# Performance work log

Hardware: AMD Instinct MI355X
Metric: run time of the kernel (lower is better)

Reference implementation:

```python
import jax, jax.numpy as jnp
import numpy as np

HIDDEN = 1024
HEADS = 16
D_K = HIDDEN // HEADS
B, S = 2, 2048


def setup_inputs() -> dict:
    key = jax.random.key(0)
    ks = jax.random.split(key, 11)
    sc = 1.0 / np.sqrt(HIDDEN)
    inp = {
        "q": jax.random.normal(ks[0], (B, S, HIDDEN), jnp.float32),
        "k": jax.random.normal(ks[1], (B, S, HIDDEN), jnp.float32),
        "v": jax.random.normal(ks[2], (B, S, HIDDEN), jnp.float32),
        "Wq": jax.random.normal(ks[3], (HIDDEN, HIDDEN), jnp.float32) * sc,
        "bq": jnp.zeros((HIDDEN,), jnp.float32),
        "Wk": jax.random.normal(ks[4], (HIDDEN, HIDDEN), jnp.float32) * sc,
        "bk": jnp.zeros((HIDDEN,), jnp.float32),
        "Wv": jax.random.normal(ks[5], (HIDDEN, HIDDEN), jnp.float32) * sc,
        "bv": jnp.zeros((HIDDEN,), jnp.float32),
        "Wo": jax.random.normal(ks[6], (HIDDEN, HIDDEN), jnp.float32) * sc,
        "bo": jnp.zeros((HIDDEN,), jnp.float32),
    }
    return inp


def reference(q, k, v, Wq, bq, Wk, bk, Wv, bv, Wo, bo):
    bs = q.shape[0]
    # projections; torch Linear: x @ W.T + b
    def proj(x, W, b):
        y = x @ W.T + b  # [B,S,H*Dk]
        return y.reshape(bs, -1, HEADS, D_K).transpose(0, 2, 1, 3)  # [B,h,S,Dk]
    qh, kh, vh = proj(q, Wq, bq), proj(k, Wk, bk), proj(v, Wv, bv)
    scores = jnp.einsum("bhqd,bhkd->bhqk", qh, kh) / jnp.sqrt(jnp.float32(D_K))
    attn = jax.nn.softmax(scores, axis=-1)  # dropout is identity in eval mode
    x = jnp.einsum("bhqk,bhkd->bhqd", attn, vh)
    x = x.transpose(0, 2, 1, 3).reshape(bs, -1, HEADS * D_K)
    return x @ Wo.T + bo
```

## Files before the change

kernel.cpp:

```cpp
#include <hip/hip_runtime.h>
#include <stdint.h>

#define HIDDEN 1024
#define HEADS  16
#define DK     64
#define BATCH  2
#define SEQ    2048
#define MTOT   (BATCH*SEQ)
#define QSCALE 0.1803368801111204f

typedef float  f32x4   __attribute__((ext_vector_type(4)));
typedef float  f32x16  __attribute__((ext_vector_type(16)));
typedef __bf16 bf16x8  __attribute__((ext_vector_type(8)));

__device__ __forceinline__ unsigned short f2bf(float f) {
    union { float f; uint32_t u; } x;
    x.f = f;
    uint32_t r = x.u + 0x7fffu + ((x.u >> 16) & 1u);
    return (unsigned short)(r >> 16);
}

__device__ __forceinline__ bf16x8 ld_bf8(const unsigned short* p) {
    return *reinterpret_cast<const bf16x8*>(p);
}

__device__ __forceinline__ void gload16(const void* g, void* l) {
    __builtin_amdgcn_global_load_lds(
        (const __attribute__((address_space(1))) void*)g,
        (__attribute__((address_space(3))) void*)l, 16, 0, 0);
}

__device__ __forceinline__ uint32_t pkbf(float a, float b) {
    union { __bf16 h[2]; uint32_t u; } pk;
    pk.h[0] = (__bf16)a; pk.h[1] = (__bf16)b;
    return pk.u;
}

struct Cvt7 {
    const float* s[7];
    unsigned short* d[7];
    int n8[7];
};
__global__ __launch_bounds__(256) void cvt_all(Cvt7 a) {
    int id = blockIdx.y;
    int i = blockIdx.x * blockDim.x + threadIdx.x;
    if (i >= a.n8[id]) return;
    const float4* s = reinterpret_cast<const float4*>(a.s[id]) + (size_t)i * 2;
    float4 x = s[0], y = s[1];
    union { unsigned short us[8]; uint4 v; } o;
    o.us[0] = f2bf(x.x); o.us[1] = f2bf(x.y); o.us[2] = f2bf(x.z); o.us[3] = f2bf(x.w);
    o.us[4] = f2bf(y.x); o.us[5] = f2bf(y.y); o.us[6] = f2bf(y.z); o.us[7] = f2bf(y.w);
    reinterpret_cast<uint4*>(a.d[id])[i] = o.v;
}

__device__ __forceinline__ void gemm_body(const unsigned short* __restrict__ A,
                                          const unsigned short* __restrict__ W,
                                          const float* __restrict__ bias,
                                          void* __restrict__ out, int mode, float scale) {
    __shared__ __align__(16) unsigned short Alds[2][128 * 64];
    __shared__ __align__(16) unsigned short Blds[2][128 * 64];
    const int t    = threadIdx.x;
    const int lane = t & 63;
    const int wid  = t >> 6;
    const int wm   = (wid >> 1) * 64;
    const int wn   = (wid & 1) * 64;
    const int fr   = lane & 15;
    const int fg   = lane >> 4;
    const int bm   = blockIdx.y, bn = blockIdx.x;
    const int K    = HIDDEN;

    f32x4 acc[4][4];
#pragma unroll
    for (int i = 0; i < 4; i++)
#pragma unroll
        for (int j = 0; j < 4; j++) acc[i][j] = (f32x4){0.f, 0.f, 0.f, 0.f};

    const int seg_row = t >> 3;
    const int seg_col = ((t & 7) ^ (seg_row & 7)) * 8;
    const int ldst    = (t & ~63) * 8;

    const unsigned short* ga = A + (size_t)(bm * 128 + seg_row) * K + seg_col;
    const unsigned short* gb = W + (size_t)(bn * 128 + seg_row) * K + seg_col;

    auto stage = [&](int k0, int buf) {
#pragma unroll
        for (int i = 0; i < 4; i++) {
            gload16(ga + (size_t)(i * 32) * K + k0, &Alds[buf][i * 2048 + ldst]);
            gload16(gb + (size_t)(i * 32) * K + k0, &Blds[buf][i * 2048 + ldst]);
        }
    };

    stage(0, 0);
    __syncthreads();

    for (int ks = 0; ks < K / 64; ++ks) {
        const int cur = ks & 1;
        if (ks < K / 64 - 1) stage((ks + 1) * 64, cur ^ 1);
#pragma unroll
        for (int kk = 0; kk < 2; kk++) {
            bf16x8 af[4], bf[4];
#pragma unroll
            for (int mt = 0; mt < 4; mt++)
                af[mt] = ld_bf8(&Alds[cur][(wm + mt * 16 + fr) * 64 +
                                           (((kk * 4 + fg) ^ (fr & 7)) * 8)]);
#pragma unroll
            for (int nt = 0; nt < 4; nt++)
                bf[nt] = ld_bf8(&Blds[cur][(wn + nt * 16 + fr) * 64 +
                                           (((kk * 4 + fg) ^ (fr & 7)) * 8)]);
#pragma unroll
            for (int mt = 0; mt < 4; mt++)
#pragma unroll
                for (int nt = 0; nt < 4; nt++)
                    acc[mt][nt] = __builtin_amdgcn_mfma_f32_16x16x32_bf16(
                        af[mt], bf[nt], acc[mt][nt], 0, 0, 0);
        }
        __syncthreads();
    }

    const int base_row = bm * 128 + wm + fg * 4;
    const int base_col = bn * 128 + wn + fr;
#pragma unroll
    for (int mt = 0; mt < 4; mt++) {
#pragma unroll
        for (int nt = 0; nt < 4; nt++) {
            int col = base_col + nt * 16;
            float bv = bias[col];
#pragma unroll
            for (int e = 0; e < 4; e++) {
                int row = base_row + mt * 16 + e;
                float val = (acc[mt][nt][e] + bv) * scale;
                if (mode == 2) {
                    ((float*)out)[(size_t)row * HIDDEN + col] = val;
                } else {
                    int b = row >> 11, s = row & (SEQ - 1);
                    int h = col >> 6, d = col & (DK - 1);
                    size_t idx;
                    if (mode == 0)
                        idx = ((size_t)(b * HEADS + h) * SEQ + s) * DK + d;
                    else
                        idx = ((size_t)(b * HEADS + h) * DK + d) * SEQ + s;
                    ((unsigned short*)out)[idx] = f2bf(val);
                }
            }
        }
    }
}

__global__ __launch_bounds__(256) void gemm_qkv(
    const unsigned short* __restrict__ qbf, const unsigned short* __restrict__ kbf,
    const unsigned short* __restrict__ vbf, const unsigned short* __restrict__ wq,
    const unsigned short* __restrict__ wk, const unsigned short* __restrict__ wv,
    const float* __restrict__ bq, const float* __restrict__ bk,
    const float* __restrict__ bv, unsigned short* __restrict__ qh,
    unsigned short* __restrict__ kh, unsigned short* __restrict__ vt) {
    int z = blockIdx.z;
    const unsigned short* A = (z == 0) ? qbf : (z == 1) ? kbf : vbf;
    const unsigned short* W = (z == 0) ? wq : (z == 1) ? wk : wv;
    const float* bias       = (z == 0) ? bq : (z == 1) ? bk : bv;
    unsigned short* out     = (z == 0) ? qh : (z == 1) ? kh : vt;
    gemm_body(A, W, bias, out, (z == 2) ? 1 : 0, (z == 0) ? QSCALE : 1.0f);
}

__global__ __launch_bounds__(256) void gemm_out(const unsigned short* __restrict__ ctx,
                                                const unsigned short* __restrict__ wo,
                                                const float* __restrict__ bo,
                                                float* __restrict__ out) {
    gemm_body(ctx, wo, bo, out, 2, 1.0f);
}

__global__ __launch_bounds__(512, 4) void attn_kernel(const unsigned short* __restrict__ qh,
                                                      const unsigned short* __restrict__ kh,
                                                      const unsigned short* __restrict__ vt,
                                                      unsigned short* __restrict__ ctx) {
    const int t = threadIdx.x, lane = t & 63, w = t >> 6;
    const int lo = lane & 31, hi = lane >> 5;
    const int qsub = w & 3, split = w >> 2;
    const int id = blockIdx.x;
    const int g  = (id & 7) * 64 + (id >> 3);
    const int by = g >> 4;
    const int bx = g & 15;
    const size_t hb = (size_t)by * (SEQ * DK);
    const int q0 = bx * 128 + qsub * 32;

    struct KV { unsigned short K[2][2][64 * 64]; unsigned short V[2][2][64 * 64]; };
    struct MG { float Lo[4][32][64]; float Lml[4][2][64]; };
    __shared__ union SMem { KV kv; MG mg; } sm;

    const unsigned short* sp[4];
    unsigned short* dpK[4];
    int sstr[4];
#pragma unroll
    for (int i = 0; i < 4; ++i) {
        int u   = w * 4 + i;
        int isV = u >> 4;
        int ssp = (u >> 3) & 1;
        int r0  = (u & 7) * 8;
        int rl  = r0 + (lane >> 3);
        int cs  = ((lane & 7) ^ ((lane >> 3) & 7)) * 8;
        if (!isV) {
            sp[i]   = kh + hb + (size_t)(ssp * 1024 + rl) * DK + cs;
            sstr[i] = 64 * DK;
            dpK[i]  = &sm.kv.K[0][ssp][r0 * 64];
        } else {
            sp[i]   = vt + hb + (size_t)rl * SEQ + ssp * 1024 + cs;
            sstr[i] = 64;
            dpK[i]  = &sm.kv.V[0][ssp][r0 * 64];
        }
    }
    const int bufoff = 2 * 64 * 64;

    bf16x8 qf[4];
#pragma unroll
    for (int tl = 0; tl < 4; ++tl)
        qf[tl] = ld_bf8(&qh[hb + (size_t)(q0 + lo) * DK + tl * 16 + hi * 8]);

    f32x16 o0, o1;
#pragma unroll
    for (int e = 0; e < 16; ++e) { o0[e] = 0.f; o1[e] = 0.f; }
    float m = -3.0e38f, l = 0.f;

#pragma unroll
    for (int i = 0; i < 4; ++i) { gload16(sp[i], dpK[i]); sp[i] += sstr[i]; }
    __syncthreads();

    const int xr = lo & 7;

    for (int it = 0; it < 16; ++it) {
        const unsigned short* Kb = &sm.kv.K[it & 1][split][0];
        const unsigned short* Vb = &sm.kv.V[it & 1][split][0];
        if (it < 15) {
#pragma unroll
            for (int i = 0; i < 4; ++i) {
                unsigned short* d = dpK[i] + ((it & 1) ? 0 : bufoff);
                gload16(sp[i], d);
                sp[i] += sstr[i];
            }
        }
        f32x16 sA, sB;
#pragma unroll
        for (int e = 0; e < 16; ++e) { sA[e] = 0.f; sB[e] = 0.f; }
        __builtin_amdgcn_s_setprio(1);
#pragma unroll
        for (int tl = 0; tl < 4; ++tl) {
            int c = 2 * tl + hi;
            bf16x8 kfA = ld_bf8(&Kb[lo * 64 + ((c ^ xr) * 8)]);
            bf16x8 kfB = ld_bf8(&Kb[(32 + lo) * 64 + ((c ^ xr) * 8)]);
            sA = __builtin_amdgcn_mfma_f32_32x32x16_bf16(kfA, qf[tl], sA, 0, 0, 0);
            sB = __builtin_amdgcn_mfma_f32_32x32x16_bf16(kfB, qf[tl], sB, 0, 0, 0);
        }
        __builtin_amdgcn_s_setprio(0);
        float pm = sA[0];
#pragma unroll
        for (int e = 1; e < 16; ++e) pm = fmaxf(pm, sA[e]);
#pragma unroll
        for (int e = 0; e < 16; ++e) pm = fmaxf(pm, sB[e]);
        pm = fmaxf(pm, __shfl_xor(pm, 32));
        if (__any(pm > m + 8.f)) {
            float mn  = fmaxf(m, pm);
            float fac = __builtin_amdgcn_exp2f(m - mn);
            m = mn;
            l *= fac;
#pragma unroll
            for (int e = 0; e < 16; ++e) { o0[e] *= fac; o1[e] *= fac; }
        }
        float sum = 0.f;
#pragma unroll
        for (int e = 0; e < 16; ++e) {
            sA[e] = __builtin_amdgcn_exp2f(sA[e] - m);
            sB[e] = __builtin_amdgcn_exp2f(sB[e] - m);
            sum += sA[e] + sB[e];
        }
        sum += __shfl_xor(sum, 32);
        l += sum;
        uint32_t pkA[8], pkB[8];
#pragma unroll
        for (int i = 0; i < 8; ++i) {
            pkA[i] = pkbf(sA[2 * i], sA[2 * i + 1]);
            pkB[i] = pkbf(sB[2 * i], sB[2 * i + 1]);
        }
        asm volatile("v_permlane32_swap_b32 %0, %1" : "+v"(pkA[0]), "+v"(pkA[2]));
        asm volatile("v_permlane32_swap_b32 %0, %1" : "+v"(pkA[1]), "+v"(pkA[3]));
        asm volatile("v_permlane32_swap_b32 %0, %1" : "+v"(pkA[4]), "+v"(pkA[6]));
        asm volatile("v_permlane32_swap_b32 %0, %1" : "+v"(pkA[5]), "+v"(pkA[7]));
        asm volatile("v_permlane32_swap_b32 %0, %1" : "+v"(pkB[0]), "+v"(pkB[2]));
        asm volatile("v_permlane32_swap_b32 %0, %1" : "+v"(pkB[1]), "+v"(pkB[3]));
        asm volatile("v_permlane32_swap_b32 %0, %1" : "+v"(pkB[4]), "+v"(pkB[6]));
        asm volatile("v_permlane32_swap_b32 %0, %1" : "+v"(pkB[5]), "+v"(pkB[7]));
        union { uint32_t u[4]; bf16x8 v; } f0, f1, f2, f3;
        f0.u[0] = pkA[0]; f0.u[1] = pkA[1]; f0.u[2] = pkA[2]; f0.u[3] = pkA[3];
        f1.u[0] = pkA[4]; f1.u[1] = pkA[5]; f1.u[2] = pkA[6]; f1.u[3] = pkA[7];
        f2.u[0] = pkB[0]; f2.u[1] = pkB[1]; f2.u[2] = pkB[2]; f2.u[3] = pkB[3];
        f3.u[0] = pkB[4]; f3.u[1] = pkB[5]; f3.u[2] = pkB[6]; f3.u[3] = pkB[7];
        bf16x8 v00 = ld_bf8(&Vb[lo * 64 + (((0 + hi) ^ xr) * 8)]);
        bf16x8 v01 = ld_bf8(&Vb[lo * 64 + (((2 + hi) ^ xr) * 8)]);
        bf16x8 v02 = ld_bf8(&Vb[lo * 64 + (((4 + hi) ^ xr) * 8)]);
        bf16x8 v03 = ld_bf8(&Vb[lo * 64 + (((6 + hi) ^ xr) * 8)]);
        bf16x8 v10 = ld_bf8(&Vb[(32 + lo) * 64 + (((0 + hi) ^ xr) * 8)]);
        bf16x8 v11 = ld_bf8(&Vb[(32 + lo) * 64 + (((2 + hi) ^ xr) * 8)]);
        bf16x8 v12 = ld_bf8(&Vb[(32 + lo) * 64 + (((4 + hi) ^ xr) * 8)]);
        bf16x8 v13 = ld_bf8(&Vb[(32 + lo) * 64 + (((6 + hi) ^ xr) * 8)]);
        __builtin_amdgcn_s_setprio(1);
        o0 = __builtin_amdgcn_mfma_f32_32x32x16_bf16(v00, f0.v, o0, 0, 0, 0);
        o0 = __builtin_amdgcn_mfma_f32_32x32x16_bf16(v01, f1.v, o0, 0, 0, 0);
        o0 = __builtin_amdgcn_mfma_f32_32x32x16_bf16(v02, f2.v, o0, 0, 0, 0);
        o0 = __builtin_amdgcn_mfma_f32_32x32x16_bf16(v03, f3.v, o0, 0, 0, 0);
        o1 = __builtin_amdgcn_mfma_f32_32x32x16_bf16(v10, f0.v, o1, 0, 0, 0);
        o1 = __builtin_amdgcn_mfma_f32_32x32x16_bf16(v11, f1.v, o1, 0, 0, 0);
        o1 = __builtin_amdgcn_mfma_f32_32x32x16_bf16(v12, f2.v, o1, 0, 0, 0);
        o1 = __builtin_amdgcn_mfma_f32_32x32x16_bf16(v13, f3.v, o1, 0, 0, 0);
        __builtin_amdgcn_s_setprio(0);
        __syncthreads();
    }

    if (split == 1) {
#pragma unroll
        for (int e = 0; e < 16; ++e) {
            sm.mg.Lo[qsub][e][lane]      = o0[e];
            sm.mg.Lo[qsub][16 + e][lane] = o1[e];
        }
        sm.mg.Lml[qsub][0][lane] = m;
        sm.mg.Lml[qsub][1][lane] = l;
    }
    __syncthreads();
    if (split == 0) {
        float m2 = sm.mg.Lml[qsub][0][lane];
        float l2 = sm.mg.Lml[qsub][1][lane];
        float M  = fmaxf(m, m2);
        float a0 = __builtin_amdgcn_exp2f(m - M);
        float a1 = __builtin_amdgcn_exp2f(m2 - M);
        float rl = __builtin_amdgcn_rcpf(a0 * l + a1 * l2);
        const int b = by >> 4, hd = by & 15;
        unsigned short* orow = ctx + ((size_t)(b * SEQ + q0 + lo)) * HIDDEN + hd * 64;
#pragma unroll
        for (int dt = 0; dt < 2; ++dt) {
#pragma unroll
            for (int gq = 0; gq < 4; ++gq) {
                union { unsigned short us[4]; uint2 v; } pk;
#pragma unroll
                for (int c = 0; c < 4; ++c) {
                    int e = gq * 4 + c;
                    float own = dt ? o1[e] : o0[e];
                    float oth = sm.mg.Lo[qsub][dt * 16 + e][lane];
                    pk.us[c] = f2bf((own * a0 + oth * a1) * rl);
                }
                *reinterpret_cast<uint2*>(orow + dt * 32 + gq * 8 + hi * 4) = pk.v;
            }
        }
    }
}

extern "C" void kernel_launch(void* const* d_in, const int* in_sizes, int n_in,
                              void* d_out, int out_size, void* d_ws, size_t ws_size,
                              hipStream_t stream) {
    const float* q  = (const float*)d_in[0];
    const float* k  = (const float*)d_in[1];
    const float* v  = (const float*)d_in[2];
    const float* Wq = (const float*)d_in[3];
    const float* bq = (const float*)d_in[4];
    const float* Wk = (const float*)d_in[5];
    const float* bk = (const float*)d_in[6];
    const float* Wv = (const float*)d_in[7];
    const float* bv = (const float*)d_in[8];
    const float* Wo = (const float*)d_in[9];
    const float* bo = (const float*)d_in[10];

    unsigned short* qbf = (unsigned short*)d_ws;
    unsigned short* kbf = qbf + (size_t)MTOT * HIDDEN;
    unsigned short* vbf = kbf + (size_t)MTOT * HIDDEN;
    unsigned short* wqb = vbf + (size_t)MTOT * HIDDEN;
    unsigned short* wkb = wqb + (size_t)HIDDEN * HIDDEN;
    unsigned short* wvb = wkb + (size_t)HIDDEN * HIDDEN;
    unsigned short* wob = wvb + (size_t)HIDDEN * HIDDEN;
    unsigned short* qh  = wob + (size_t)HIDDEN * HIDDEN;
    unsigned short* kh  = qh + (size_t)MTOT * HIDDEN;
    unsigned short* vt  = kh + (size_t)MTOT * HIDDEN;
    unsigned short* ctx = vt + (size_t)MTOT * HIDDEN;

    const int nAct8 = MTOT * HIDDEN / 8;
    const int nW8   = HIDDEN * HIDDEN / 8;

    Cvt7 ca;
    ca.s[0] = q;  ca.d[0] = qbf; ca.n8[0] = nAct8;
    ca.s[1] = k;  ca.d[1] = kbf; ca.n8[1] = nAct8;
    ca.s[2] = v;  ca.d[2] = vbf; ca.n8[2] = nAct8;
    ca.s[3] = Wq; ca.d[3] = wqb; ca.n8[3] = nW8;
    ca.s[4] = Wk; ca.d[4] = wkb; ca.n8[4] = nW8;
    ca.s[5] = Wv; ca.d[5] = wvb; ca.n8[5] = nW8;
    ca.s[6] = Wo; ca.d[6] = wob; ca.n8[6] = nW8;
    cvt_all<<<dim3(nAct8 / 256, 7), dim3(256), 0, stream>>>(ca);

    gemm_qkv<<<dim3(HIDDEN / 128, MTOT / 128, 3), dim3(256), 0, stream>>>(
        qbf, kbf, vbf, wqb, wkb, wvb, bq, bk, bv, qh, kh, vt);

    attn_kernel<<<dim3(512), dim3(512), 0, stream>>>(qh, kh, vt, ctx);

    gemm_out<<<dim3(HIDDEN / 128, MTOT / 128), dim3(256), 0, stream>>>(
        ctx, wob, bo, (float*)d_out);
}
```

Before: 147.8 us.

## Process two query tiles per warp in attention to reuse K/V fragments

Each attention warp now handles two 32-row query tiles (256 queries per block instead of 128), reusing every K and V fragment read from shared memory for both tiles. The grid is halved to 256 blocks, the launch-bounds occupancy hint drops from 4 to 2 to allow the extra accumulators, and the two softmax/PV phases are interleaved for overlap. Max and sum reductions are rewritten as balanced trees. This cuts LDS traffic and K/V global loads per query, at the cost of higher register pressure, lower occupancy, and fewer blocks than the 256 CUs can comfortably overlap.

```diff
diff --git a/kernel.cpp b/kernel.cpp
--- a/kernel.cpp
+++ b/kernel.cpp
@@ -34,6 +34,22 @@
     union { __bf16 h[2]; uint32_t u; } pk;
     pk.h[0] = (__bf16)a; pk.h[1] = (__bf16)b;
     return pk.u;
+}
+
+__device__ __forceinline__ float tmax16(const f32x16& v) {
+    float a = fmaxf(fmaxf(v[0], v[1]), fmaxf(v[2], v[3]));
+    float b = fmaxf(fmaxf(v[4], v[5]), fmaxf(v[6], v[7]));
+    float c = fmaxf(fmaxf(v[8], v[9]), fmaxf(v[10], v[11]));
+    float d = fmaxf(fmaxf(v[12], v[13]), fmaxf(v[14], v[15]));
+    return fmaxf(fmaxf(a, b), fmaxf(c, d));
+}
+
+__device__ __forceinline__ float tsum16(const f32x16& v) {
+    float a = (v[0] + v[1]) + (v[2] + v[3]);
+    float b = (v[4] + v[5]) + (v[6] + v[7]);
+    float c = (v[8] + v[9]) + (v[10] + v[11]);
+    float d = (v[12] + v[13]) + (v[14] + v[15]);
+    return (a + b) + (c + d);
 }
 
 struct Cvt7 {
@@ -168,7 +184,7 @@
     gemm_body(ctx, wo, bo, out, 2, 1.0f);
 }
 
-__global__ __launch_bounds__(512, 4) void attn_kernel(const unsigned short* __restrict__ qh,
+__global__ __launch_bounds__(512, 2) void attn_kernel(const unsigned short* __restrict__ qh,
                                                       const unsigned short* __restrict__ kh,
                                                       const unsigned short* __restrict__ vt,
                                                       unsigned short* __restrict__ ctx) {
@@ -176,14 +192,15 @@
     const int lo = lane & 31, hi = lane >> 5;
     const int qsub = w & 3, split = w >> 2;
     const int id = blockIdx.x;
-    const int g  = (id & 7) * 64 + (id >> 3);
-    const int by = g >> 4;
-    const int bx = g & 15;
+    const int g  = (id & 7) * 32 + (id >> 3);
+    const int by = g >> 3;
+    const int bx = g & 7;
     const size_t hb = (size_t)by * (SEQ * DK);
-    const int q0 = bx * 128 + qsub * 32;
+    const int q0a = bx * 256 + qsub * 32;
+    const int q0b = q0a + 128;
 
     struct KV { unsigned short K[2][2][64 * 64]; unsigned short V[2][2][64 * 64]; };
-    struct MG { float Lo[4][32][64]; float Lml[4][2][64]; };
+    struct MG { float Lo[4][2][32][64]; float Lml[4][2][2][64]; };
     __shared__ union SMem { KV kv; MG mg; } sm;
 
     const unsigned short* sp[4];
@@ -209,15 +226,17 @@
     }
     const int bufoff = 2 * 64 * 64;
 
-    bf16x8 qf[4];
-#pragma unroll
-    for (int tl = 0; tl < 4; ++tl)
-        qf[tl] = ld_bf8(&qh[hb + (size_t)(q0 + lo) * DK + tl * 16 + hi * 8]);
-
-    f32x16 o0, o1;
-#pragma unroll
-    for (int e = 0; e < 16; ++e) { o0[e] = 0.f; o1[e] = 0.f; }
-    float m = -3.0e38f, l = 0.f;
+    bf16x8 qfA[4], qfB[4];
+#pragma unroll
+    for (int tl = 0; tl < 4; ++tl) {
+        qfA[tl] = ld_bf8(&qh[hb + (size_t)(q0a + lo) * DK + tl * 16 + hi * 8]);
+        qfB[tl] = ld_bf8(&qh[hb + (size_t)(q0b + lo) * DK + tl * 16 + hi * 8]);
+    }
+
+    f32x16 o0a, o1a, o0b, o1b;
+#pragma unroll
+    for (int e = 0; e < 16; ++e) { o0a[e] = 0.f; o1a[e] = 0.f; o0b[e] = 0.f; o1b[e] = 0.f; }
+    float mA = -3.0e38f, lA = 0.f, mB = -3.0e38f, lB = 0.f;
 
 #pragma unroll
     for (int i = 0; i < 4; ++i) { gload16(sp[i], dpK[i]); sp[i] += sstr[i]; }
@@ -236,61 +255,60 @@
                 sp[i] += sstr[i];
             }
         }
-        f32x16 sA, sB;
-#pragma unroll
-        for (int e = 0; e < 16; ++e) { sA[e] = 0.f; sB[e] = 0.f; }
+        f32x16 sAa, sBa, sAb, sBb;
+#pragma unroll
+        for (int e = 0; e < 16; ++e) { sAa[e] = 0.f; sBa[e] = 0.f; sAb[e] = 0.f; sBb[e] = 0.f; }
         __builtin_amdgcn_s_setprio(1);
 #pragma unroll
         for (int tl = 0; tl < 4; ++tl) {
             int c = 2 * tl + hi;
             bf16x8 kfA = ld_bf8(&Kb[lo * 64 + ((c ^ xr) * 8)]);
             bf16x8 kfB = ld_bf8(&Kb[(32 + lo) * 64 + ((c ^ xr) * 8)]);
-            sA = __builtin_amdgcn_mfma_f32_32x32x16_bf16(kfA, qf[tl], sA, 0, 0, 0);
-            sB = __builtin_amdgcn_mfma_f32_32x32x16_bf16(kfB, qf[tl], sB, 0, 0, 0);
+            sAa = __builtin_amdgcn_mfma_f32_32x32x16_bf16(kfA, qfA[tl], sAa, 0, 0, 0);
+            sBa = __builtin_amdgcn_mfma_f32_32x32x16_bf16(kfB, qfA[tl], sBa, 0, 0, 0);
+            sAb = __builtin_amdgcn_mfma_f32_32x32x16_bf16(kfA, qfB[tl], sAb, 0, 0, 0);
+            sBb = __builtin_amdgcn_mfma_f32_32x32x16_bf16(kfB, qfB[tl], sBb, 0, 0, 0);
         }
         __builtin_amdgcn_s_setprio(0);
-        float pm = sA[0];
-#pragma unroll
-        for (int e = 1; e < 16; ++e) pm = fmaxf(pm, sA[e]);
-#pragma unroll
-        for (int e = 0; e < 16; ++e) pm = fmaxf(pm, sB[e]);
+        float pm = fmaxf(tmax16(sAa), tmax16(sBa));
         pm = fmaxf(pm, __shfl_xor(pm, 32));
-        if (__any(pm > m + 8.f)) {
-            float mn  = fmaxf(m, pm);
-            float fac = __builtin_amdgcn_exp2f(m - mn);
-            m = mn;
-            l *= fac;
-#pragma unroll
-            for (int e = 0; e < 16; ++e) { o0[e] *= fac; o1[e] *= fac; }
-        }
-        float sum = 0.f;
+        if (__any(pm > mA + 8.f)) {
+            float mn  = fmaxf(mA, pm);
+            float fac = __builtin_amdgcn_exp2f(mA - mn);
+            mA = mn;
+            lA *= fac;
+#pragma unroll
+            for (int e = 0; e < 16; ++e) { o0a[e] *= fac; o1a[e] *= fac; }
+        }
 #pragma unroll
         for (int e = 0; e < 16; ++e) {
-            sA[e] = __builtin_amdgcn_exp2f(sA[e] - m);
-            sB[e] = __builtin_amdgcn_exp2f(sB[e] - m);
-            sum += sA[e] + sB[e];
-        }
-        sum += __shfl_xor(sum, 32);
-        l += sum;
-        uint32_t pkA[8], pkB[8];
+            sAa[e] = __builtin_amdgcn_exp2f(sAa[e] - mA);
+            sBa[e] = __builtin_amdgcn_exp2f(sBa[e] - mA);
+        }
+        {
+            float sum = tsum16(sAa) + tsum16(sBa);
+            sum += __shfl_xor(sum, 32);
+            lA += sum;
+        }
+        uint32_t pA[8], pB[8];
 #pragma unroll
         for (int i = 0; i < 8; ++i) {
-            pkA[i] = pkbf(sA[2 * i], sA[2 * i + 1]);
-            pkB[i] = pkbf(sB[2 * i], sB[2 * i + 1]);
-        }
-        asm volatile("v_permlane32_swap_b32 %0, %1" : "+v"(pkA[0]), "+v"(pkA[2]));
-        asm volatile("v_permlane32_swap_b32 %0, %1" : "+v"(pkA[1]), "+v"(pkA[3]));
-        asm volatile("v_permlane32_swap_b32 %0, %1" : "+v"(pkA[4]), "+v"(pkA[6]));
-        asm volatile("v_permlane32_swap_b32 %0, %1" : "+v"(pkA[5]), "+v"(pkA[7]));
-        asm volatile("v_permlane32_swap_b32 %0, %1" : "+v"(pkB[0]), "+v"(pkB[2]));
-        asm volatile("v_permlane32_swap_b32 %0, %1" : "+v"(pkB[1]), "+v"(pkB[3]));
-        asm volatile("v_permlane32_swap_b32 %0, %1" : "+v"(pkB[4]), "+v"(pkB[6]));
-        asm volatile("v_permlane32_swap_b32 %0, %1" : "+v"(pkB[5]), "+v"(pkB[7]));
-        union { uint32_t u[4]; bf16x8 v; } f0, f1, f2, f3;
-        f0.u[0] = pkA[0]; f0.u[1] = pkA[1]; f0.u[2] = pkA[2]; f0.u[3] = pkA[3];
-        f1.u[0] = pkA[4]; f1.u[1] = pkA[5]; f1.u[2] = pkA[6]; f1.u[3] = pkA[7];
-        f2.u[0] = pkB[0]; f2.u[1] = pkB[1]; f2.u[2] = pkB[2]; f2.u[3] = pkB[3];
-        f3.u[0] = pkB[4]; f3.u[1] = pkB[5]; f3.u[2] = pkB[6]; f3.u[3] = pkB[7];
+            pA[i] = pkbf(sAa[2 * i], sAa[2 * i + 1]);
+            pB[i] = pkbf(sBa[2 * i], sBa[2 * i + 1]);
+        }
+        asm volatile("v_permlane32_swap_b32 %0, %1" : "+v"(pA[0]), "+v"(pA[2]));
+        asm volatile("v_permlane32_swap_b32 %0, %1" : "+v"(pA[1]), "+v"(pA[3]));
+        asm volatile("v_permlane32_swap_b32 %0, %1" : "+v"(pA[4]), "+v"(pA[6]));
+        asm volatile("v_permlane32_swap_b32 %0, %1" : "+v"(pA[5]), "+v"(pA[7]));
+        asm volatile("v_permlane32_swap_b32 %0, %1" : "+v"(pB[0]), "+v"(pB[2]));
+        asm volatile("v_permlane32_swap_b32 %0, %1" : "+v"(pB[1]), "+v"(pB[3]));
+        asm volatile("v_permlane32_swap_b32 %0, %1" : "+v"(pB[4]), "+v"(pB[6]));
+        asm volatile("v_permlane32_swap_b32 %0, %1" : "+v"(pB[5]), "+v"(pB[7]));
+        union { uint32_t u[4]; bf16x8 v; } f0a, f1a, f2a, f3a;
+        f0a.u[0] = pA[0]; f0a.u[1] = pA[1]; f0a.u[2] = pA[2]; f0a.u[3] = pA[3];
+        f1a.u[0] = pA[4]; f1a.u[1] = pA[5]; f1a.u[2] = pA[6]; f1a.u[3] = pA[7];
+        f2a.u[0] = pB[0]; f2a.u[1] = pB[1]; f2a.u[2] = pB[2]; f2a.u[3] = pB[3];
+        f3a.u[0] = pB[4]; f3a.u[1] = pB[5]; f3a.u[2] = pB[6]; f3a.u[3] = pB[7];
         bf16x8 v00 = ld_bf8(&Vb[lo * 64 + (((0 + hi) ^ xr) * 8)]);
         bf16x8 v01 = ld_bf8(&Vb[lo * 64 + (((2 + hi) ^ xr) * 8)]);
         bf16x8 v02 = ld_bf8(&Vb[lo * 64 + (((4 + hi) ^ xr) * 8)]);
@@ -300,14 +318,62 @@
         bf16x8 v12 = ld_bf8(&Vb[(32 + lo) * 64 + (((4 + hi) ^ xr) * 8)]);
         bf16x8 v13 = ld_bf8(&Vb[(32 + lo) * 64 + (((6 + hi) ^ xr) * 8)]);
         __builtin_amdgcn_s_setprio(1);
-        o0 = __builtin_amdgcn_mfma_f32_32x32x16_bf16(v00, f0.v, o0, 0, 0, 0);
-        o0 = __builtin_amdgcn_mfma_f32_32x32x16_bf16(v01, f1.v, o0, 0, 0, 0);
-        o0 = __builtin_amdgcn_mfma_f32_32x32x16_bf16(v02, f2.v, o0, 0, 0, 0);
-        o0 = __builtin_amdgcn_mfma_f32_32x32x16_bf16(v03, f3.v, o0, 0, 0, 0);
-        o1 = __builtin_amdgcn_mfma_f32_32x32x16_bf16(v10, f0.v, o1, 0, 0, 0);
-        o1 = __builtin_amdgcn_mfma_f32_32x32x16_bf16(v11, f1.v, o1, 0, 0, 0);
-        o1 = __builtin_amdgcn_mfma_f32_32x32x16_bf16(v12, f2.v, o1, 0, 0, 0);
-        o1 = __builtin_amdgcn_mfma_f32_32x32x16_bf16(v13, f3.v, o1, 0, 0, 0);
+        o0a = __builtin_amdgcn_mfma_f32_32x32x16_bf16(v00, f0a.v, o0a, 0, 0, 0);
+        o0a = __builtin_amdgcn_mfma_f32_32x32x16_bf16(v01, f1a.v, o0a, 0, 0, 0);
+        o0a = __builtin_amdgcn_mfma_f32_32x32x16_bf16(v02, f2a.v, o0a, 0, 0, 0);
+        o0a = __builtin_amdgcn_mfma_f32_32x32x16_bf16(v03, f3a.v, o0a, 0, 0, 0);
+        o1a = __builtin_amdgcn_mfma_f32_32x32x16_bf16(v10, f0a.v, o1a, 0, 0, 0);
+        o1a = __builtin_amdgcn_mfma_f32_32x32x16_bf16(v11, f1a.v, o1a, 0, 0, 0);
+        o1a = __builtin_amdgcn_mfma_f32_32x32x16_bf16(v12, f2a.v, o1a, 0, 0, 0);
+        o1a = __builtin_amdgcn_mfma_f32_32x32x16_bf16(v13, f3a.v, o1a, 0, 0, 0);
+        __builtin_amdgcn_s_setprio(0);
+        float qm = fmaxf(tmax16(sAb), tmax16(sBb));
+        qm = fmaxf(qm, __shfl_xor(qm, 32));
+        if (__any(qm > mB + 8.f)) {
+            float mn  = fmaxf(mB, qm);
+            float fac = __builtin_amdgcn_exp2f(mB - mn);
+            mB = mn;
+            lB *= fac;
+#pragma unroll
+            for (int e = 0; e < 16; ++e) { o0b[e] *= fac; o1b[e] *= fac; }
+        }
+#pragma unroll
+        for (int e = 0; e < 16; ++e) {
+            sAb[e] = __builtin_amdgcn_exp2f(sAb[e] - mB);
+            sBb[e] = __builtin_amdgcn_exp2f(sBb[e] - mB);
+        }
+        {
+            float sum = tsum16(sAb) + tsum16(sBb);
+            sum += __shfl_xor(sum, 32);
+            lB += sum;
+        }
+#pragma unroll
+        for (int i = 0; i < 8; ++i) {
+            pA[i] = pkbf(sAb[2 * i], sAb[2 * i + 1]);
+            pB[i] = pkbf(sBb[2 * i], sBb[2 * i + 1]);
+        }
+        asm volatile("v_permlane32_swap_b32 %0, %1" : "+v"(pA[0]), "+v"(pA[2]));
+        asm volatile("v_permlane32_swap_b32 %0, %1" : "+v"(pA[1]), "+v"(pA[3]));
+        asm volatile("v_permlane32_swap_b32 %0, %1" : "+v"(pA[4]), "+v"(pA[6]));
+        asm volatile("v_permlane32_swap_b32 %0, %1" : "+v"(pA[5]), "+v"(pA[7]));
+        asm volatile("v_permlane32_swap_b32 %0, %1" : "+v"(pB[0]), "+v"(pB[2]));
+        asm volatile("v_permlane32_swap_b32 %0, %1" : "+v"(pB[1]), "+v"(pB[3]));
+        asm volatile("v_permlane32_swap_b32 %0, %1" : "+v"(pB[4]), "+v"(pB[6]));
+        asm volatile("v_permlane32_swap_b32 %0, %1" : "+v"(pB[5]), "+v"(pB[7]));
+        union { uint32_t u[4]; bf16x8 v; } f0b, f1b, f2b, f3b;
+        f0b.u[0] = pA[0]; f0b.u[1] = pA[1]; f0b.u[2] = pA[2]; f0b.u[3] = pA[3];
+        f1b.u[0] = pA[4]; f1b.u[1] = pA[5]; f1b.u[2] = pA[6]; f1b.u[3] = pA[7];
+        f2b.u[0] = pB[0]; f2b.u[1] = pB[1]; f2b.u[2] = pB[2]; f2b.u[3] = pB[3];
+        f3b.u[0] = pB[4]; f3b.u[1] = pB[5]; f3b.u[2] = pB[6]; f3b.u[3] = pB[7];
+        __builtin_amdgcn_s_setprio(1);
+        o0b = __builtin_amdgcn_mfma_f32_32x32x16_bf16(v00, f0b.v, o0b, 0, 0, 0);
+        o0b = __builtin_amdgcn_mfma_f32_32x32x16_bf16(v01, f1b.v, o0b, 0, 0, 0);
+        o0b = __builtin_amdgcn_mfma_f32_32x32x16_bf16(v02, f2b.v, o0b, 0, 0, 0);
+        o0b = __builtin_amdgcn_mfma_f32_32x32x16_bf16(v03, f3b.v, o0b, 0, 0, 0);
+        o1b = __builtin_amdgcn_mfma_f32_32x32x16_bf16(v10, f0b.v, o1b, 0, 0, 0);
+        o1b = __builtin_amdgcn_mfma_f32_32x32x16_bf16(v11, f1b.v, o1b, 0, 0, 0);
+        o1b = __builtin_amdgcn_mfma_f32_32x32x16_bf16(v12, f2b.v, o1b, 0, 0, 0);
+        o1b = __builtin_amdgcn_mfma_f32_32x32x16_bf16(v13, f3b.v, o1b, 0, 0, 0);
         __builtin_amdgcn_s_setprio(0);
         __syncthreads();
     }
@@ -315,35 +381,65 @@
     if (split == 1) {
 #pragma unroll
         for (int e = 0; e < 16; ++e) {
-            sm.mg.Lo[qsub][e][lane]      = o0[e];
-            sm.mg.Lo[qsub][16 + e][lane] = o1[e];
-        }
-        sm.mg.Lml[qsub][0][lane] = m;
-        sm.mg.Lml[qsub][1][lane] = l;
+            sm.mg.Lo[qsub][0][e][lane]      = o0a[e];
+            sm.mg.Lo[qsub][0][16 + e][lane] = o1a[e];
+            sm.mg.Lo[qsub][1][e][lane]      = o0b[e];
+            sm.mg.Lo[qsub][1][16 + e][lane] = o1b[e];
+        }
+        sm.mg.Lml[qsub][0][0][lane] = mA;
+        sm.mg.Lml[qsub][0][1][lane] = lA;
+        sm.mg.Lml[qsub][1][0][lane] = mB;
+        sm.mg.Lml[qsub][1][1][lane] = lB;
     }
     __syncthreads();
     if (split == 0) {
-        float m2 = sm.mg.Lml[qsub][0][lane];
-        float l2 = sm.mg.Lml[qsub][1][lane];
-        float M  = fmaxf(m, m2);
-        float a0 = __builtin_amdgcn_exp2f(m - M);
-        float a1 = __builtin_amdgcn_exp2f(m2 - M);
-        float rl = __builtin_amdgcn_rcpf(a0 * l + a1 * l2);
         const int b = by >> 4, hd = by & 15;
-        unsigned short* orow = ctx + ((size_t)(b * SEQ + q0 + lo)) * HIDDEN + hd * 64;
-#pragma unroll
-        for (int dt = 0; dt < 2; ++dt) {
-#pragma unroll
-            for (int gq = 0; gq < 4; ++gq) {
-                union { unsigned short us[4]; uint2 v; } pk;
-#pragma unroll
-                for (int c = 0; c < 4; ++c) {
-                    int e = gq * 4 + c;
-                    float own = dt ? o1[e] : o0[e];
-                    float oth = sm.mg.Lo[qsub][dt * 16 + e][lane];
-                    pk.us[c] = f2bf((own * a0 + oth * a1) * rl);
+        {
+            float m2 = sm.mg.Lml[qsub][0][0][lane];
+            float l2 = sm.mg.Lml[qsub][0][1][lane];
+            float M  = fmaxf(mA, m2);
+            float a0 = __builtin_amdgcn_exp2f(mA - M);
+            float a1 = __builtin_amdgcn_exp2f(m2 - M);
+            float rl = __builtin_amdgcn_rcpf(a0 * lA + a1 * l2);
+            unsigned short* orow = ctx + ((size_t)(b * SEQ + q0a + lo)) * HIDDEN + hd * 64;
+#pragma unroll
+            for (int dt = 0; dt < 2; ++dt) {
+#pragma unroll
+                for (int gq = 0; gq < 4; ++gq) {
+                    union { unsigned short us[4]; uint2 v; } pk;
+#pragma unroll
+                    for (int c = 0; c < 4; ++c) {
+                        int e = gq * 4 + c;
+                        float own = dt ? o1a[e] : o0a[e];
+                        float oth = sm.mg.Lo[qsub][0][dt * 16 + e][lane];
+                        pk.us[c] = f2bf((own * a0 + oth * a1) * rl);
+                    }
+                    *reinterpret_cast<uint2*>(orow + dt * 32 + gq * 8 + hi * 4) = pk.v;
                 }
-                *reinterpret_cast<uint2*>(orow + dt * 32 + gq * 8 + hi * 4) = pk.v;
+            }
+        }
+        {
+            float m2 = sm.mg.Lml[qsub][1][0][lane];
+            float l2 = sm.mg.Lml[qsub][1][1][lane];
+            float M  = fmaxf(mB, m2);
+            float a0 = __builtin_amdgcn_exp2f(mB - M);
+            float a1 = __builtin_amdgcn_exp2f(m2 - M);
+            float rl = __builtin_amdgcn_rcpf(a0 * lB + a1 * l2);
+            unsigned short* orow = ctx + ((size_t)(b * SEQ + q0b + lo)) * HIDDEN + hd * 64;
+#pragma unroll
+            for (int dt = 0; dt < 2; ++dt) {
+#pragma unroll
+                for (int gq = 0; gq < 4; ++gq) {
+                    union { unsigned short us[4]; uint2 v; } pk;
+#pragma unroll
+                    for (int c = 0; c < 4; ++c) {
+                        int e = gq * 4 + c;
+                        float own = dt ? o1b[e] : o0b[e];
+                        float oth = sm.mg.Lo[qsub][1][dt * 16 + e][lane];
+                        pk.us[c] = f2bf((own * a0 + oth * a1) * rl);
+                    }
+                    *reinterpret_cast<uint2*>(orow + dt * 32 + gq * 8 + hi * 4) = pk.v;
+                }
             }
         }
     }
@@ -392,7 +488,7 @@
     gemm_qkv<<<dim3(HIDDEN / 128, MTOT / 128, 3), dim3(256), 0, stream>>>(
         qbf, kbf, vbf, wqb, wkb, wvb, bq, bk, bv, qh, kh, vt);
 
-    attn_kernel<<<dim3(512), dim3(512), 0, stream>>>(qh, kh, vt, ctx);
+    attn_kernel<<<dim3(256), dim3(512), 0, stream>>>(qh, kh, vt, ctx);
 
     gemm_out<<<dim3(HIDDEN / 128, MTOT / 128), dim3(256), 0, stream>>>(
         ctx, wob, bo, (float*)d_out);
```

Measured after the change: 147.2 us. Within noise of the previous version (-0.4%).
